# Kernel optimization log

Hardware: AMD Instinct MI355X
Metric: run time of the kernel (lower is better)

## Reference

```python
import jax, jax.numpy as jnp
import numpy as np
from math import sqrt

B, S, D, H = 4, 2048, 1024, 16
DH = D // H          # 64
DF = 4 * D           # 4096
EPS = 1e-5
NEG = -1e9


def layer_norm(x, w, b):
    mu = jnp.mean(x, axis=-1, keepdims=True)
    var = jnp.mean((x - mu) ** 2, axis=-1, keepdims=True)
    return (x - mu) * jax.lax.rsqrt(var + EPS) * w + b


def setup_inputs() -> dict:
    key = jax.random.key(0)
    ks = jax.random.split(key, 16)
    s = 0.02
    return {
        "state": jax.random.normal(ks[0], (B, S, D), jnp.float32),
        "mask": jax.random.randint(ks[1], (B, S), 0, 2, jnp.int32),
        "ln1_w": jnp.ones((D,), jnp.float32),
        "ln1_b": jnp.zeros((D,), jnp.float32),
        "Wq": jax.random.normal(ks[2], (H, D, DH), jnp.float32) * s,
        "bq": jnp.zeros((H, DH), jnp.float32),
        "Wk": jax.random.normal(ks[3], (H, D, DH), jnp.float32) * s,
        "bk": jnp.zeros((H, DH), jnp.float32),
        "Wv": jax.random.normal(ks[4], (H, D, DH), jnp.float32) * s,
        "bv": jnp.zeros((H, DH), jnp.float32),
        "Wo": jax.random.normal(ks[5], (D, D), jnp.float32) * s,
        "bo": jnp.zeros((D,), jnp.float32),
        "ln2_w": jnp.ones((D,), jnp.float32),
        "ln2_b": jnp.zeros((D,), jnp.float32),
        "W1": jax.random.normal(ks[6], (D, DF), jnp.float32) * s,
        "b1": jnp.zeros((DF,), jnp.float32),
        "W2": jax.random.normal(ks[7], (DF, D), jnp.float32) * s,
        "b2": jnp.zeros((D,), jnp.float32),
    }


def reference(state, mask, ln1_w, ln1_b, Wq, bq, Wk, bk, Wv, bv, Wo, bo,
              ln2_w, ln2_b, W1, b1, W2, b2):
    # pre-norm attention block
    hidden = layer_norm(state, ln1_w, ln1_b)               # [B,S,D]
    q = jnp.einsum("bsd,hde->bhse", hidden, Wq) + bq[None, :, None, :]
    k = jnp.einsum("bsd,hde->bhse", hidden, Wk) + bk[None, :, None, :]
    v = jnp.einsum("bsd,hde->bhse", hidden, Wv) + bv[None, :, None, :]
    scores = jnp.einsum("bhse,bhte->bhst", q, k) / sqrt(DH)  # [B,H,S,S]
    scores = jnp.where(mask[:, None, None, :] == 0, NEG, scores)
    weights = jax.nn.softmax(scores, axis=-1)
    attended = jnp.einsum("bhst,bhte->bhse", weights, v)    # [B,H,S,DH]
    # concat heads in head order (matches torch cat over per-head outputs)
    attended = attended.transpose(0, 2, 1, 3).reshape(B, S, D)
    attn_out = attended @ Wo + bo
    output = state + attn_out
    # pre-norm FFN block (dropout=0 -> identity)
    hidden = layer_norm(output, ln2_w, ln2_b)
    ff = jax.nn.gelu(hidden @ W1 + b1, approximate=False) @ W2 + b2
    return output + ff
```

## Files before the change

kernel.cpp:

```cpp
#include <hip/hip_runtime.h>
#include <math.h>

#define B_  4
#define S_  2048
#define D_  1024
#define H_  16
#define DH_ 64
#define DF_ 4096
#define M_  8192

#define QSC 0.18033688011112042f

typedef __attribute__((ext_vector_type(8))) short bf8_t;
typedef __attribute__((ext_vector_type(4))) float f4_t;

#if defined(__has_builtin)
#if __has_builtin(__builtin_amdgcn_cvt_pk_bf16_f32)
#define HAVE_PKCVT 1
#endif
#if __has_builtin(__builtin_amdgcn_global_load_lds)
#define HAVE_ASYNC 1
#endif
#if __has_builtin(__builtin_amdgcn_exp2f)
#define EXP2F(x) __builtin_amdgcn_exp2f(x)
#else
#define EXP2F(x) __expf((x) * 0.69314718055994531f)
#endif
#else
#define EXP2F(x) __expf((x) * 0.69314718055994531f)
#endif

__device__ __forceinline__ unsigned pk_bf16(float lo, float hi) {
#ifdef HAVE_PKCVT
  auto r = __builtin_amdgcn_cvt_pk_bf16_f32(lo, hi);
  unsigned u; __builtin_memcpy(&u, &r, 4); return u;
#else
  union { float f; unsigned u; } a, b2; a.f = lo; b2.f = hi;
  unsigned ra = a.u + 0x7fffu + ((a.u >> 16) & 1u);
  unsigned rb = b2.u + 0x7fffu + ((b2.u >> 16) & 1u);
  return (ra >> 16) | (rb & 0xffff0000u);
#endif
}

__device__ __forceinline__ unsigned short f2bf(float x) {
  return (unsigned short)(pk_bf16(x, x) & 0xffffu);
}

__device__ __forceinline__ bf8_t upk8(unsigned u0, unsigned u1, unsigned u2, unsigned u3) {
  union { unsigned u[4]; bf8_t v; } c;
  c.u[0] = u0; c.u[1] = u1; c.u[2] = u2; c.u[3] = u3; return c.v;
}

__device__ __forceinline__ f4_t mfma32(bf8_t a, bf8_t b, f4_t c) {
  return __builtin_amdgcn_mfma_f32_16x16x32_bf16(a, b, c, 0, 0, 0);
}

__device__ __forceinline__ void async16(const void* g, void* l) {
#ifdef HAVE_ASYNC
  __builtin_amdgcn_global_load_lds((__attribute__((address_space(1))) void*)(g),
                                   (__attribute__((address_space(3))) void*)(l), 16, 0, 0);
#else
  *(uint4*)l = *(const uint4*)g;
#endif
}

__device__ __forceinline__ int sw(int row) { return row & 7; }


__global__ __launch_bounds__(256) void wtrans_kernel(const float* __restrict__ in,
                                                     unsigned short* __restrict__ out,
                                                     int K, int N) {
  const int k0 = blockIdx.x * 32, n0 = blockIdx.y * 32;
  __shared__ float t[32][33];
  const int tid = threadIdx.x;
#pragma unroll
  for (int i = 0; i < 4; i++) {
    int idx = i * 256 + tid; int r = idx >> 5, c = idx & 31;
    t[r][c] = in[(size_t)(k0 + r) * N + n0 + c];
  }
  __syncthreads();
#pragma unroll
  for (int i = 0; i < 4; i++) {
    int idx = i * 256 + tid; int r = idx >> 5, c = idx & 31;
    out[(size_t)(n0 + r) * K + k0 + c] = f2bf(t[c][r]);
  }
}

__global__ __launch_bounds__(256) void qkvpack_kernel(const float* __restrict__ Wq,
                                                      const float* __restrict__ Wk,
                                                      const float* __restrict__ Wv,
                                                      unsigned short* __restrict__ WqkvT) {
  const int z = blockIdx.z;
  const int sel = z >> 4, h = z & 15;
  const float* in = (sel == 0 ? Wq : sel == 1 ? Wk : Wv) + (size_t)h * D_ * DH_;
  const int k0 = blockIdx.x * 32, n0 = blockIdx.y * 32;
  __shared__ float t[32][33];
  const int tid = threadIdx.x;
#pragma unroll
  for (int i = 0; i < 4; i++) {
    int idx = i * 256 + tid; int r = idx >> 5, c = idx & 31;
    t[r][c] = in[(size_t)(k0 + r) * DH_ + n0 + c];
  }
  __syncthreads();
#pragma unroll
  for (int i = 0; i < 4; i++) {
    int idx = i * 256 + tid; int r = idx >> 5, c = idx & 31;
    int n = sel * 1024 + h * 64 + n0 + r;
    WqkvT[(size_t)n * D_ + k0 + c] = f2bf(t[c][r]);
  }
}

__global__ void biaspack_kernel(const float* __restrict__ bq, const float* __restrict__ bk,
                                const float* __restrict__ bv, float* __restrict__ bqkv) {
  int i = blockIdx.x * 256 + threadIdx.x;
  if (i < 3072) {
    int sel = i >> 10, j = i & 1023;
    const float* src = sel == 0 ? bq : sel == 1 ? bk : bv;
    bqkv[i] = src[j];
  }
}


__global__ __launch_bounds__(256) void ln_kernel(const float* __restrict__ x,
                                                 const float* __restrict__ w,
                                                 const float* __restrict__ bb,
                                                 unsigned short* __restrict__ out) {
  const int row = blockIdx.x;
  const float* xr = x + (size_t)row * D_;
  const int tid = threadIdx.x;
  float v[4]; float s = 0.f;
#pragma unroll
  for (int i = 0; i < 4; i++) { v[i] = xr[tid + i * 256]; s += v[i]; }
  __shared__ float red[8];
#pragma unroll
  for (int o = 32; o; o >>= 1) s += __shfl_xor(s, o, 64);
  const int wv = tid >> 6, ln = tid & 63;
  if (!ln) red[wv] = s;
  __syncthreads();
  float mean = (red[0] + red[1] + red[2] + red[3]) * (1.f / 1024.f);
  float s2 = 0.f;
#pragma unroll
  for (int i = 0; i < 4; i++) { float d = v[i] - mean; s2 += d * d; }
#pragma unroll
  for (int o = 32; o; o >>= 1) s2 += __shfl_xor(s2, o, 64);
  if (!ln) red[4 + wv] = s2;
  __syncthreads();
  float var = (red[4] + red[5] + red[6] + red[7]) * (1.f / 1024.f);
  float rstd = rsqrtf(var + 1e-5f);
#pragma unroll
  for (int i = 0; i < 4; i++) {
    int c = tid + i * 256;
    out[(size_t)row * D_ + c] = f2bf((v[i] - mean) * rstd * w[c] + bb[c]);
  }
}

__global__ __launch_bounds__(256) void ffn2red_kernel(float* __restrict__ out,
                                                      const float* __restrict__ P,
                                                      const float* __restrict__ resid,
                                                      const float* __restrict__ bias) {
  const size_t i = ((size_t)blockIdx.x * 256 + threadIdx.x) * 4;
  f4_t a  = *(const f4_t*)&out[i];
  f4_t p  = *(const f4_t*)&P[i];
  f4_t rr = *(const f4_t*)&resid[i];
  f4_t bb = *(const f4_t*)&bias[(int)(i & 1023)];
  *(f4_t*)&out[i] = a + p + rr + bb;
}

template <int EPI>
__global__ __launch_bounds__(256) void gemm_bt(const unsigned short* __restrict__ A,
                                               const unsigned short* __restrict__ Bt,
                                               const float* __restrict__ bias,
                                               const float* __restrict__ resid,
                                               unsigned short* __restrict__ outb,
                                               float* __restrict__ outf,
                                               int Ndim, int Kdim) {
  __shared__ __align__(16) unsigned short Asmem[4096];
  __shared__ __align__(16) unsigned short Bsmem[4096];
  const int tid = threadIdx.x;
  const int wave = tid >> 6, lane = tid & 63;
  const int quad = lane >> 4, l16 = lane & 15;
  const int wm = wave >> 1, wn = wave & 1;

  const int gx = gridDim.x;
  const int nwg = gx * (int)gridDim.y;
  const int lin = (int)blockIdx.y * gx + (int)blockIdx.x;
  const int swz = (lin & 7) * (nwg >> 3) + (lin >> 3);
  const int m0 = (swz / gx) * 128, n0 = (swz % gx) * 128;

  const f4_t fzero = {0.f, 0.f, 0.f, 0.f};
  f4_t acc[4][4];
#pragma unroll
  for (int i = 0; i < 4; i++)
#pragma unroll
    for (int j = 0; j < 4; j++) acc[i][j] = fzero;

  const int rowA = tid >> 2;
  const int kp = (tid & 3) * 8;

  for (int k0 = 0; k0 < Kdim; k0 += 32) {
    __syncthreads();
#pragma unroll
    for (int r = 0; r < 2; r++) {
      const int row = r * 64 + rowA;
      const int e = row * 32 + kp;
      async16(A  + (size_t)(m0 + row) * Kdim + k0 + kp, &Asmem[e]);
      async16(Bt + (size_t)(n0 + row) * Kdim + k0 + kp, &Bsmem[e]);
    }
    __syncthreads();

    bf8_t a[4], b[4];
#pragma unroll
    for (int i = 0; i < 4; i++) {
      a[i] = *(const bf8_t*)&Asmem[(wm * 64 + i * 16 + l16) * 32 + quad * 8];
      b[i] = *(const bf8_t*)&Bsmem[(wn * 64 + i * 16 + l16) * 32 + quad * 8];
    }
#pragma unroll
    for (int i = 0; i < 4; i++)
#pragma unroll
      for (int j = 0; j < 4; j++)
        acc[i][j] = mfma32(a[i], b[j], acc[i][j]);
  }

#pragma unroll
  for (int i = 0; i < 4; i++) {
#pragma unroll
    for (int j = 0; j < 4; j++) {
#pragma unroll
      for (int r = 0; r < 4; r++) {
        const int m = m0 + wm * 64 + i * 16 + quad * 4 + r;
        const int n = n0 + wn * 64 + j * 16 + l16;
        float v = acc[i][j][r] + bias[n];
        if constexpr (EPI == 2) v = 0.5f * v * (1.f + erff(v * 0.70710678118654752f));
        if constexpr (EPI == 1) {
          v += resid[(size_t)m * Ndim + n];
          outf[(size_t)m * Ndim + n] = v;
        } else {
          outb[(size_t)m * Ndim + n] = f2bf(v);
        }
      }
    }
  }
}

template <int EPI>
__global__ __launch_bounds__(512, 2) void gemm256(const unsigned short* __restrict__ A,
                                                  const unsigned short* __restrict__ Bt,
                                                  const float* __restrict__ bias,
                                                  const float* __restrict__ resid,
                                                  unsigned short* __restrict__ outb,
                                                  float* __restrict__ outf,
                                                  float* __restrict__ outf2,
                                                  unsigned short* __restrict__ vTout,
                                                  int Ndim, int Kdim, int Kstride) {
  __shared__ __align__(16) unsigned short Asm[32768];
  __shared__ __align__(16) unsigned short Bsm[32768];
  const int tid = threadIdx.x;
  const int wave = tid >> 6, lane = tid & 63;
  const int quad = lane >> 4, l16 = lane & 15;
  const int wm = wave >> 2, wn = wave & 3;

  const int gx = gridDim.x;
  const int nwg = gx * (int)gridDim.y;
  const int lin = (int)blockIdx.y * gx + (int)blockIdx.x;
  const int swz = (lin & 7) * (nwg >> 3) + (lin >> 3);
  const int m0 = (swz / gx) * 256, n0 = (swz % gx) * 256;
  const int kz = (int)blockIdx.z * Kdim;

  const int NT = Kdim >> 6;
  const int srow = lane >> 3, schk = lane & 7;

#define STAGE_A(t, row0) do {                                               \
    const int r_ = (row0) + srow;                                           \
    async16(A + (size_t)(m0 + r_) * Kstride + kz + (t) * 64 +               \
                ((schk ^ (r_ & 7)) << 3),                                   \
            &Asm[(((t) & 1) << 14) + ((row0) << 6)]); } while (0)
#define STAGE_B(t, row0) do {                                               \
    const int r_ = (row0) + srow;                                           \
    async16(Bt + (size_t)(n0 + r_) * Kstride + kz + (t) * 64 +              \
                 ((schk ^ (r_ & 7)) << 3),                                  \
            &Bsm[(((t) & 1) << 14) + ((row0) << 6)]); } while (0)
#define STAGE_A0(t) do { STAGE_A(t, wave * 8); STAGE_A(t, 128 + wave * 8); } while (0)
#define STAGE_A1(t) do { STAGE_A(t, 64 + wave * 8); STAGE_A(t, 192 + wave * 8); } while (0)
#define STAGE_B0(t) do { const int rb_ = (wave >> 1) * 64 + (wave & 1) * 8;  \
    STAGE_B(t, rb_); STAGE_B(t, rb_ + 16); } while (0)
#define STAGE_B1(t) do { const int rb_ = (wave >> 1) * 64 + 32 + (wave & 1) * 8; \
    STAGE_B(t, rb_); STAGE_B(t, rb_ + 16); } while (0)

#define AFR(bo, row, s) \
  (*(const bf8_t*)&Asm[(bo) + ((row) << 6) + ((((s) * 4 + quad) ^ ((row) & 7)) << 3)])
#define BFR(bo, row, s) \
  (*(const bf8_t*)&Bsm[(bo) + ((row) << 6) + ((((s) * 4 + quad) ^ ((row) & 7)) << 3)])

  const f4_t fzero = {0.f, 0.f, 0.f, 0.f};
  f4_t acc[8][4];
#pragma unroll
  for (int i = 0; i < 8; i++)
#pragma unroll
    for (int j = 0; j < 4; j++) acc[i][j] = fzero;

  STAGE_A0(0); STAGE_A1(0); STAGE_B0(0); STAGE_B1(0);
  STAGE_A0(1); STAGE_A1(1); STAGE_B0(1); STAGE_B1(1);
  asm volatile("s_waitcnt vmcnt(8)" ::: "memory");
  __builtin_amdgcn_s_barrier();

  const int ar0 = wm << 7;
  const int br0 = wn << 6;

  for (int t = 0; t < NT; ++t) {
    const int bo = (t & 1) << 14;
    const bool pf = (t + 2) < NT;
    const int t2 = t + 2;
    bf8_t af[4][2], bf0[2][2], bf1[2][2];

#pragma unroll
    for (int i = 0; i < 4; i++) {
      af[i][0] = AFR(bo, ar0 + i * 16 + l16, 0);
      af[i][1] = AFR(bo, ar0 + i * 16 + l16, 1);
    }
#pragma unroll
    for (int j = 0; j < 2; j++) {
      bf0[j][0] = BFR(bo, br0 + j * 16 + l16, 0);
      bf0[j][1] = BFR(bo, br0 + j * 16 + l16, 1);
    }
    asm volatile("s_waitcnt lgkmcnt(8)" ::: "memory");
    __builtin_amdgcn_s_barrier();
    asm volatile("s_waitcnt lgkmcnt(0)" ::: "memory");
    __builtin_amdgcn_sched_barrier(0);
    __builtin_amdgcn_s_setprio(1);
#pragma unroll
    for (int s = 0; s < 2; s++)
#pragma unroll
      for (int i = 0; i < 4; i++)
#pragma unroll
        for (int j = 0; j < 2; j++)
          acc[i][j] = mfma32(af[i][s], bf0[j][s], acc[i][j]);
    __builtin_amdgcn_s_setprio(0);
    __builtin_amdgcn_s_barrier();

#pragma unroll
    for (int j = 0; j < 2; j++) {
      bf1[j][0] = BFR(bo, br0 + 32 + j * 16 + l16, 0);
      bf1[j][1] = BFR(bo, br0 + 32 + j * 16 + l16, 1);
    }
    if (pf) { STAGE_A0(t2); STAGE_B0(t2); }
    __builtin_amdgcn_s_barrier();
    asm volatile("s_waitcnt lgkmcnt(0)" ::: "memory");
    __builtin_amdgcn_sched_barrier(0);
    __builtin_amdgcn_s_setprio(1);
#pragma unroll
    for (int s = 0; s < 2; s++)
#pragma unroll
      for (int i = 0; i < 4; i++)
#pragma unroll
        for (int j = 0; j < 2; j++)
          acc[i][2 + j] = mfma32(af[i][s], bf1[j][s], acc[i][2 + j]);
    __builtin_amdgcn_s_setprio(0);
    __builtin_amdgcn_s_barrier();

#pragma unroll
    for (int i = 0; i < 4; i++) {
      af[i][0] = AFR(bo, ar0 + 64 + i * 16 + l16, 0);
      af[i][1] = AFR(bo, ar0 + 64 + i * 16 + l16, 1);
    }
    if (pf) STAGE_B1(t2);
    __builtin_amdgcn_s_barrier();
    asm volatile("s_waitcnt lgkmcnt(0)" ::: "memory");
    __builtin_amdgcn_sched_barrier(0);
    __builtin_amdgcn_s_setprio(1);
#pragma unroll
    for (int s = 0; s < 2; s++)
#pragma unroll
      for (int i = 0; i < 4; i++)
#pragma unroll
        for (int j = 0; j < 2; j++)
          acc[4 + i][2 + j] = mfma32(af[i][s], bf1[j][s], acc[4 + i][2 + j]);
    __builtin_amdgcn_s_setprio(0);
    __builtin_amdgcn_s_barrier();

    if (pf) STAGE_A1(t2);
    __builtin_amdgcn_s_barrier();
    __builtin_amdgcn_s_setprio(1);
#pragma unroll
    for (int s = 0; s < 2; s++)
#pragma unroll
      for (int i = 0; i < 4; i++)
#pragma unroll
        for (int j = 0; j < 2; j++)
          acc[4 + i][j] = mfma32(af[i][s], bf0[j][s], acc[4 + i][j]);
    __builtin_amdgcn_s_setprio(0);
    if (pf) asm volatile("s_waitcnt vmcnt(8)" ::: "memory");
    else    asm volatile("s_waitcnt vmcnt(0)" ::: "memory");
    __builtin_amdgcn_s_barrier();
  }

#undef STAGE_A
#undef STAGE_B
#undef STAGE_A0
#undef STAGE_A1
#undef STAGE_B0
#undef STAGE_B1
#undef AFR
#undef BFR

  if (EPI == 0 && n0 >= 2048) {
    const int bb2 = m0 >> 11;
    const int sb64 = (m0 & 2047) + (wm << 7);
#pragma unroll
    for (int mi = 0; mi < 8; mi++) {
      const int i4 = mi & 3;
      const int g0 = (i4 & 2) * 16 + 8 * quad + 4 * (i4 & 1);
      const int sbase = sb64 + (mi >> 2) * 64 + g0;
#pragma unroll
      for (int nj = 0; nj < 4; nj++) {
        const int n = n0 + wn * 64 + nj * 16 + l16;
        const int ef = n - 2048;
        const int hh = ef >> 6, e = ef & 63;
        const float bsv = bias[n];
        uint2 wq;
        wq.x = pk_bf16(acc[mi][nj][0] + bsv, acc[mi][nj][1] + bsv);
        wq.y = pk_bf16(acc[mi][nj][2] + bsv, acc[mi][nj][3] + bsv);
        *(uint2*)&vTout[(size_t)((bb2 * 16 + hh) * 64 + e) * S_ + sbase] = wq;
      }
    }
    return;
  }

  float* const pdst = (EPI == 3) ? (blockIdx.z ? outf2 : outf) : outf;
  const float sc = (EPI == 0 && n0 < 1024) ? QSC : 1.f;
#pragma unroll
  for (int mi = 0; mi < 8; mi++) {
#pragma unroll
    for (int nj = 0; nj < 4; nj++) {
      const int n = n0 + wn * 64 + nj * 16 + l16;
      const float bs = (EPI == 3) ? 0.f : bias[n];
#pragma unroll
      for (int r = 0; r < 4; r++) {
        const int m = m0 + wm * 128 + mi * 16 + quad * 4 + r;
        float v = acc[mi][nj][r] + bs;
        if constexpr (EPI == 0) v *= sc;
        if constexpr (EPI == 2) v = 0.5f * v * (1.f + erff(v * 0.70710678118654752f));
        if constexpr (EPI == 1) {
          v += resid[(size_t)m * Ndim + n];
          outf[(size_t)m * Ndim + n] = v;
        } else if constexpr (EPI == 3) {
          pdst[(size_t)m * Ndim + n] = v;
        } else {
          outb[(size_t)m * Ndim + n] = f2bf(v);
        }
      }
    }
  }
}


__global__ __launch_bounds__(256) void attn_kernel(const unsigned short* __restrict__ qkv,
                                                   const unsigned short* __restrict__ vT,
                                                   const int* __restrict__ maskp,
                                                   unsigned short* __restrict__ attended) {
  const int bh = blockIdx.y, b = bh >> 4, h = bh & 15;
  const int q0 = blockIdx.x * 128;
  const int tid = threadIdx.x, wv = tid >> 6, lane = tid & 63;
  const int quad = lane >> 4, l16 = lane & 15;
  __shared__ __align__(16) unsigned short smem[16384];
  __shared__ float biasl[128];
  unsigned short* Ks = smem;
  unsigned short* Vs = smem + 8192;

  bf8_t aq[2][2];
#pragma unroll
  for (int sb = 0; sb < 2; sb++) {
    const unsigned short* qrow =
        qkv + (size_t)(b * S_ + q0 + wv * 32 + sb * 16 + l16) * 3072 + h * 64;
    aq[sb][0] = *(const bf8_t*)(qrow + quad * 8);
    aq[sb][1] = *(const bf8_t*)(qrow + 32 + quad * 8);
  }

  const bf8_t ones8 = {0x3F80, 0x3F80, 0x3F80, 0x3F80, 0x3F80, 0x3F80, 0x3F80, 0x3F80};
  const f4_t fzero = {0.f, 0.f, 0.f, 0.f};
  f4_t o[2][4], lacc[2];
#pragma unroll
  for (int sb = 0; sb < 2; sb++) {
    lacc[sb] = fzero;
#pragma unroll
    for (int ee = 0; ee < 4; ee++) o[sb][ee] = fzero;
  }

  for (int t0 = 0; t0 < S_; t0 += 128) {
    __syncthreads();
#pragma unroll
    for (int r = 0; r < 4; r++) {
      int ci = r * 256 + tid;
      int krow = ci >> 3, kc = (ci & 7) ^ sw(krow);
      async16(qkv + (size_t)(b * S_ + t0 + krow) * 3072 + 1024 + h * 64 + kc * 8,
              &Ks[ci * 8]);
      int e = ci >> 4, half = (ci >> 3) & 1, vc = (ci & 7) ^ sw(e);
      async16(vT + (size_t)(bh * 64 + e) * S_ + t0 + half * 64 + vc * 8,
              &Vs[ci * 8]);
    }
    if (tid < 128) biasl[tid] = maskp[b * S_ + t0 + tid] ? 0.f : -8e9f;
    __syncthreads();

#pragma unroll
    for (int th = 0; th < 2; th++) {
      f4_t sf[2][4];
#pragma unroll
      for (int jj = 0; jj < 4; jj++) {
        f4_t bi = *(const f4_t*)&biasl[th * 64 + jj * 16 + quad * 4];
        sf[0][jj] = bi;
        sf[1][jj] = bi;
      }
#pragma unroll
      for (int jj = 0; jj < 4; jj++) {
        int krow = th * 64 + jj * 16 + l16, sk = sw(krow);
        bf8_t kf0 = *(const bf8_t*)&Ks[krow * 64 + (quad ^ sk) * 8];
        bf8_t kf1 = *(const bf8_t*)&Ks[krow * 64 + ((quad + 4) ^ sk) * 8];
        sf[0][jj] = mfma32(kf0, aq[0][0], sf[0][jj]);
        sf[0][jj] = mfma32(kf1, aq[0][1], sf[0][jj]);
        sf[1][jj] = mfma32(kf0, aq[1][0], sf[1][jj]);
        sf[1][jj] = mfma32(kf1, aq[1][1], sf[1][jj]);
      }

      bf8_t pp[2][2];
#pragma unroll
      for (int sb = 0; sb < 2; sb++) {
#pragma unroll
        for (int h2 = 0; h2 < 2; h2++) {
          float p0 = EXP2F(sf[sb][2 * h2][0]),     p1 = EXP2F(sf[sb][2 * h2][1]);
          float p2 = EXP2F(sf[sb][2 * h2][2]),     p3 = EXP2F(sf[sb][2 * h2][3]);
          float p4 = EXP2F(sf[sb][2 * h2 + 1][0]), p5 = EXP2F(sf[sb][2 * h2 + 1][1]);
          float p6 = EXP2F(sf[sb][2 * h2 + 1][2]), p7 = EXP2F(sf[sb][2 * h2 + 1][3]);
          pp[sb][h2] = upk8(pk_bf16(p0, p1), pk_bf16(p2, p3),
                            pk_bf16(p4, p5), pk_bf16(p6, p7));
        }
        lacc[sb] = mfma32(ones8, pp[sb][0], lacc[sb]);
        lacc[sb] = mfma32(ones8, pp[sb][1], lacc[sb]);
      }

#pragma unroll
      for (int ee = 0; ee < 4; ee++) {
        int vrow = ee * 16 + l16, sv = sw(vrow);
#pragma unroll
        for (int h2 = 0; h2 < 2; h2++) {
          bf8_t vf = *(const bf8_t*)&Vs[vrow * 128 + th * 64 + ((4 * h2 + quad) ^ sv) * 8];
          o[0][ee] = mfma32(vf, pp[0][h2], o[0][ee]);
          o[1][ee] = mfma32(vf, pp[1][h2], o[1][ee]);
        }
      }
    }
  }

  float linv[2];
#pragma unroll
  for (int sb = 0; sb < 2; sb++) linv[sb] = 1.f / lacc[sb][0];

  __syncthreads();
  unsigned short* Os = smem;
#pragma unroll
  for (int sb = 0; sb < 2; sb++) {
    int srow = wv * 32 + sb * 16 + l16;
#pragma unroll
    for (int ee = 0; ee < 4; ee++) {
      unsigned w0 = pk_bf16(o[sb][ee][0] * linv[sb], o[sb][ee][1] * linv[sb]);
      unsigned w1 = pk_bf16(o[sb][ee][2] * linv[sb], o[sb][ee][3] * linv[sb]);
      uint2 wq; wq.x = w0; wq.y = w1;
      *(uint2*)&Os[srow * 72 + ee * 16 + quad * 4] = wq;
    }
  }
  __syncthreads();
#pragma unroll
  for (int it = 0; it < 4; it++) {
    int row = it * 32 + (tid >> 3), e0 = (tid & 7) * 8;
    bf8_t v = *(const bf8_t*)&Os[row * 72 + e0];
    *(bf8_t*)&attended[(size_t)(b * S_ + q0 + row) * D_ + h * 64 + e0] = v;
  }
}


extern "C" void kernel_launch(void* const* d_in, const int* in_sizes, int n_in,
                              void* d_out, int out_size, void* d_ws, size_t ws_size,
                              hipStream_t stream) {
  const float* state = (const float*)d_in[0];
  const int*   maskp = (const int*)d_in[1];
  const float* ln1w  = (const float*)d_in[2];
  const float* ln1b  = (const float*)d_in[3];
  const float* Wq    = (const float*)d_in[4];
  const float* bq    = (const float*)d_in[5];
  const float* Wk    = (const float*)d_in[6];
  const float* bk    = (const float*)d_in[7];
  const float* Wv    = (const float*)d_in[8];
  const float* bv    = (const float*)d_in[9];
  const float* Wo    = (const float*)d_in[10];
  const float* bo    = (const float*)d_in[11];
  const float* ln2w  = (const float*)d_in[12];
  const float* ln2b  = (const float*)d_in[13];
  const float* W1    = (const float*)d_in[14];
  const float* b1    = (const float*)d_in[15];
  const float* W2    = (const float*)d_in[16];
  const float* b2    = (const float*)d_in[17];

  char* w = (char*)d_ws;
  unsigned short* hidden = (unsigned short*)w; w += (size_t)M_ * D_ * 2;
  unsigned short* WqkvT  = (unsigned short*)w; w += (size_t)3072 * D_ * 2;
  unsigned short* WoT    = (unsigned short*)w; w += (size_t)D_ * D_ * 2;
  unsigned short* W1T    = (unsigned short*)w; w += (size_t)DF_ * D_ * 2;
  unsigned short* qkv    = (unsigned short*)w; w += (size_t)M_ * 3072 * 2;
  unsigned short* vT     = (unsigned short*)w; w += (size_t)M_ * D_ * 2;
  float*          outp   = (float*)w;          w += (size_t)M_ * D_ * 4;
  unsigned short* W2T    = (unsigned short*)w; w += (size_t)D_ * DF_ * 2;
  float*          bqkv   = (float*)w;          w += 3072 * 4;
  unsigned short* ff1    = qkv;
  float*          Pbuf   = (float*)hidden;

  qkvpack_kernel<<<dim3(32, 2, 48), 256, 0, stream>>>(Wq, Wk, Wv, WqkvT);
  wtrans_kernel<<<dim3(32, 32), 256, 0, stream>>>(Wo, WoT, D_, D_);
  wtrans_kernel<<<dim3(32, 128), 256, 0, stream>>>(W1, W1T, D_, DF_);
  wtrans_kernel<<<dim3(128, 32), 256, 0, stream>>>(W2, W2T, DF_, D_);
  biaspack_kernel<<<12, 256, 0, stream>>>(bq, bk, bv, bqkv);

  ln_kernel<<<M_, 256, 0, stream>>>(state, ln1w, ln1b, hidden);
  gemm256<0><<<dim3(3072 / 256, M_ / 256), 512, 0, stream>>>(
      hidden, WqkvT, bqkv, nullptr, qkv, nullptr, nullptr, vT, 3072, D_, D_);
  attn_kernel<<<dim3(S_ / 128, B_ * H_), 256, 0, stream>>>(qkv, vT, maskp, hidden);
  gemm_bt<1><<<dim3(D_ / 128, M_ / 128), 256, 0, stream>>>(hidden, WoT, bo, state,
                                                           nullptr, outp, D_, D_);
  ln_kernel<<<M_, 256, 0, stream>>>(outp, ln2w, ln2b, hidden);
  gemm256<2><<<dim3(DF_ / 256, M_ / 256), 512, 0, stream>>>(
      hidden, W1T, b1, nullptr, ff1, nullptr, nullptr, nullptr, DF_, D_, D_);
  gemm256<3><<<dim3(D_ / 256, M_ / 256, 2), 512, 0, stream>>>(
      ff1, W2T, nullptr, nullptr, nullptr, Pbuf, (float*)d_out, nullptr,
      D_, DF_ / 2, DF_);
  ffn2red_kernel<<<(M_ * D_) / 1024, 256, 0, stream>>>((float*)d_out, Pbuf, outp, b2);
}
```

Before: 570.4 us.

## Simplify GEMM main loop to two K-halves with single full-tile prefetch

Replaces the four-phase ping-pong GEMM inner loop, which interleaved partial LDS fragment loads, partial async prefetches and many barriers, with a simpler schedule. Each iteration now loads all A/B fragments for both K sub-steps up front, runs the first half of the MFMAs, takes one barrier, issues the whole next-tile async copy at once, then runs the second half. This cuts barrier count and scheduling complexity. In exchange it needs more live fragment registers and gives up the fine-grained interleaving of global loads with MFMA phases.

```diff
diff --git a/kernel.cpp b/kernel.cpp
--- a/kernel.cpp
+++ b/kernel.cpp
@@ -279,12 +279,11 @@
     async16(Bt + (size_t)(n0 + r_) * Kstride + kz + (t) * 64 +              \
                  ((schk ^ (r_ & 7)) << 3),                                  \
             &Bsm[(((t) & 1) << 14) + ((row0) << 6)]); } while (0)
-#define STAGE_A0(t) do { STAGE_A(t, wave * 8); STAGE_A(t, 128 + wave * 8); } while (0)
-#define STAGE_A1(t) do { STAGE_A(t, 64 + wave * 8); STAGE_A(t, 192 + wave * 8); } while (0)
-#define STAGE_B0(t) do { const int rb_ = (wave >> 1) * 64 + (wave & 1) * 8;  \
-    STAGE_B(t, rb_); STAGE_B(t, rb_ + 16); } while (0)
-#define STAGE_B1(t) do { const int rb_ = (wave >> 1) * 64 + 32 + (wave & 1) * 8; \
-    STAGE_B(t, rb_); STAGE_B(t, rb_ + 16); } while (0)
+#define STAGE_FULL(t) do {                                                  \
+    STAGE_A(t, wave * 8);       STAGE_A(t, 64 + wave * 8);                  \
+    STAGE_A(t, 128 + wave * 8); STAGE_A(t, 192 + wave * 8);                 \
+    STAGE_B(t, wave * 8);       STAGE_B(t, 64 + wave * 8);                  \
+    STAGE_B(t, 128 + wave * 8); STAGE_B(t, 192 + wave * 8); } while (0)
 
 #define AFR(bo, row, s) \
   (*(const bf8_t*)&Asm[(bo) + ((row) << 6) + ((((s) * 4 + quad) ^ ((row) & 7)) << 3)])
@@ -298,8 +297,8 @@
 #pragma unroll
     for (int j = 0; j < 4; j++) acc[i][j] = fzero;
 
-  STAGE_A0(0); STAGE_A1(0); STAGE_B0(0); STAGE_B1(0);
-  STAGE_A0(1); STAGE_A1(1); STAGE_B0(1); STAGE_B1(1);
+  STAGE_FULL(0);
+  STAGE_FULL(1);
   asm volatile("s_waitcnt vmcnt(8)" ::: "memory");
   __builtin_amdgcn_s_barrier();
 
@@ -310,84 +309,38 @@
     const int bo = (t & 1) << 14;
     const bool pf = (t + 2) < NT;
     const int t2 = t + 2;
-    bf8_t af[4][2], bf0[2][2], bf1[2][2];
-
-#pragma unroll
-    for (int i = 0; i < 4; i++) {
-      af[i][0] = AFR(bo, ar0 + i * 16 + l16, 0);
-      af[i][1] = AFR(bo, ar0 + i * 16 + l16, 1);
-    }
-#pragma unroll
-    for (int j = 0; j < 2; j++) {
-      bf0[j][0] = BFR(bo, br0 + j * 16 + l16, 0);
-      bf0[j][1] = BFR(bo, br0 + j * 16 + l16, 1);
-    }
-    asm volatile("s_waitcnt lgkmcnt(8)" ::: "memory");
+    bf8_t a0[8], b0[4], a1[8], b1[4];
+
+#pragma unroll
+    for (int i = 0; i < 8; i++) a0[i] = AFR(bo, ar0 + i * 16 + l16, 0);
+#pragma unroll
+    for (int j = 0; j < 4; j++) b0[j] = BFR(bo, br0 + j * 16 + l16, 0);
+#pragma unroll
+    for (int i = 0; i < 8; i++) a1[i] = AFR(bo, ar0 + i * 16 + l16, 1);
+#pragma unroll
+    for (int j = 0; j < 4; j++) b1[j] = BFR(bo, br0 + j * 16 + l16, 1);
+
+    __builtin_amdgcn_s_setprio(1);
+#pragma unroll
+    for (int i = 0; i < 8; i++)
+#pragma unroll
+      for (int j = 0; j < 4; j++)
+        acc[i][j] = mfma32(a0[i], b0[j], acc[i][j]);
+    __builtin_amdgcn_s_setprio(0);
+
+    asm volatile("s_waitcnt lgkmcnt(0)" ::: "memory");
     __builtin_amdgcn_s_barrier();
-    asm volatile("s_waitcnt lgkmcnt(0)" ::: "memory");
-    __builtin_amdgcn_sched_barrier(0);
+
+    if (pf) STAGE_FULL(t2);
+
     __builtin_amdgcn_s_setprio(1);
 #pragma unroll
-    for (int s = 0; s < 2; s++)
-#pragma unroll
-      for (int i = 0; i < 4; i++)
-#pragma unroll
-        for (int j = 0; j < 2; j++)
-          acc[i][j] = mfma32(af[i][s], bf0[j][s], acc[i][j]);
+    for (int i = 0; i < 8; i++)
+#pragma unroll
+      for (int j = 0; j < 4; j++)
+        acc[i][j] = mfma32(a1[i], b1[j], acc[i][j]);
     __builtin_amdgcn_s_setprio(0);
-    __builtin_amdgcn_s_barrier();
-
-#pragma unroll
-    for (int j = 0; j < 2; j++) {
-      bf1[j][0] = BFR(bo, br0 + 32 + j * 16 + l16, 0);
-      bf1[j][1] = BFR(bo, br0 + 32 + j * 16 + l16, 1);
-    }
-    if (pf) { STAGE_A0(t2); STAGE_B0(t2); }
-    __builtin_amdgcn_s_barrier();
-    asm volatile("s_waitcnt lgkmcnt(0)" ::: "memory");
-    __builtin_amdgcn_sched_barrier(0);
-    __builtin_amdgcn_s_setprio(1);
-#pragma unroll
-    for (int s = 0; s < 2; s++)
-#pragma unroll
-      for (int i = 0; i < 4; i++)
-#pragma unroll
-        for (int j = 0; j < 2; j++)
-          acc[i][2 + j] = mfma32(af[i][s], bf1[j][s], acc[i][2 + j]);
-    __builtin_amdgcn_s_setprio(0);
-    __builtin_amdgcn_s_barrier();
-
-#pragma unroll
-    for (int i = 0; i < 4; i++) {
-      af[i][0] = AFR(bo, ar0 + 64 + i * 16 + l16, 0);
-      af[i][1] = AFR(bo, ar0 + 64 + i * 16 + l16, 1);
-    }
-    if (pf) STAGE_B1(t2);
-    __builtin_amdgcn_s_barrier();
-    asm volatile("s_waitcnt lgkmcnt(0)" ::: "memory");
-    __builtin_amdgcn_sched_barrier(0);
-    __builtin_amdgcn_s_setprio(1);
-#pragma unroll
-    for (int s = 0; s < 2; s++)
-#pragma unroll
-      for (int i = 0; i < 4; i++)
-#pragma unroll
-        for (int j = 0; j < 2; j++)
-          acc[4 + i][2 + j] = mfma32(af[i][s], bf1[j][s], acc[4 + i][2 + j]);
-    __builtin_amdgcn_s_setprio(0);
-    __builtin_amdgcn_s_barrier();
-
-    if (pf) STAGE_A1(t2);
-    __builtin_amdgcn_s_barrier();
-    __builtin_amdgcn_s_setprio(1);
-#pragma unroll
-    for (int s = 0; s < 2; s++)
-#pragma unroll
-      for (int i = 0; i < 4; i++)
-#pragma unroll
-        for (int j = 0; j < 2; j++)
-          acc[4 + i][j] = mfma32(af[i][s], bf0[j][s], acc[4 + i][j]);
-    __builtin_amdgcn_s_setprio(0);
+
     if (pf) asm volatile("s_waitcnt vmcnt(8)" ::: "memory");
     else    asm volatile("s_waitcnt vmcnt(0)" ::: "memory");
     __builtin_amdgcn_s_barrier();
@@ -395,10 +348,7 @@
 
 #undef STAGE_A
 #undef STAGE_B
-#undef STAGE_A0
-#undef STAGE_A1
-#undef STAGE_B0
-#undef STAGE_B1
+#undef STAGE_FULL
 #undef AFR
 #undef BFR
 
```

Measured after the change: 550.4 us. 1.04x faster.
